# Performance work log

Hardware: AMD Instinct MI355X
Metric: run time of the kernel (lower is better)

The kernel has to match this reference:

```python
import jax, jax.numpy as jnp
import numpy as np
from jax import lax

N_KERNELS = 10000
KS = 9
DILATIONS = (1, 2, 4, 8, 16)   # static dilation groups, 2000 kernels each
GROUP = N_KERNELS // len(DILATIONS)
BN_EPS = 1e-5


def setup_inputs() -> dict:
    key = jax.random.key(0)
    kx, kw, kb, klw = jax.random.split(key, 4)
    B, L, C, n_class = 16, 256, 3, 10
    x_enc = jax.random.normal(kx, (B, L, C), dtype=jnp.float32)
    # ROCKET kernels: normal weights, mean-centered per kernel
    W = jax.random.normal(kw, (N_KERNELS, C, KS), dtype=jnp.float32)
    W = W - W.mean(axis=(1, 2), keepdims=True)
    # ROCKET biases: uniform(-1, 1)
    b = jax.random.uniform(kb, (N_KERNELS,), dtype=jnp.float32) * 2.0 - 1.0
    gamma = jnp.ones((2 * N_KERNELS,), dtype=jnp.float32)
    beta = jnp.zeros((2 * N_KERNELS,), dtype=jnp.float32)
    linW = jax.random.normal(klw, (2 * N_KERNELS, n_class), dtype=jnp.float32) * 0.01
    linB = jnp.zeros((n_class,), dtype=jnp.float32)
    return {"x_enc": x_enc, "W": W, "b": b, "gamma": gamma, "beta": beta,
            "linW": linW, "linB": linB}


def _rocket_features(x, W, b):
    # x: [B, C, L]; W: [N_KERNELS, C, KS]; b: [N_KERNELS]
    feats = []
    dn = ("NCH", "OIH", "NCH")
    for i, d in enumerate(DILATIONS):
        w = W[i * GROUP:(i + 1) * GROUP]                       # [G, C, KS]
        bb = b[i * GROUP:(i + 1) * GROUP]                      # [G]
        y = lax.conv_general_dilated(x, w, window_strides=(1,),
                                     padding="SAME", rhs_dilation=(d,),
                                     dimension_numbers=dn)      # [B, G, L]
        y = y + bb[None, :, None]
        feats.append(y.max(axis=-1))                            # max pooling
        feats.append(jnp.where(y > 0, 1.0, 0.0).mean(axis=-1))  # PPV
    return jnp.concatenate(feats, axis=-1)                      # [B, 2*N_KERNELS]


def reference(x_enc, W, b, gamma, beta, linW, linB):
    x = jnp.transpose(x_enc, (0, 2, 1))        # [B, C, L]
    feat = _rocket_features(x, W, b)           # [B, 20000]
    # BatchNorm1d (training mode: batch statistics, biased variance)
    mu = feat.mean(axis=0)
    var = feat.var(axis=0)
    feat_n = (feat - mu) * lax.rsqrt(var + BN_EPS) * gamma + beta
    return feat_n @ linW + linB                # [B, num_class]
```

## Files before the change

kernel.cpp:

```cpp
#include <hip/hip_runtime.h>
#include <cmath>

#define NK       10000
#define GROUP    2000
#define SEQ_L    256
#define FEAT_DIM 20000
#define NBATCH   16

__launch_bounds__(256)
__global__ void rocket_feat(const float* __restrict__ x_enc,
                            const float* __restrict__ Wk,
                            const float* __restrict__ bias,
                            float* __restrict__ feat)
{
    __shared__ __align__(16) float xs[1152];
    __shared__ float4 red[4][64];

    const int gi   = blockIdx.x >> 4;
    const int sb   = blockIdx.x & 15;
    const int b    = blockIdx.y;
    const int d    = 1 << gi;
    const int Mlen = (SEQ_L >> gi) + 8;
    const int tid  = threadIdx.x;
    const int lane = tid & 63;
    const int wv   = __builtin_amdgcn_readfirstlane(tid >> 6);

    const int dml = d * Mlen;
    for (int idx = tid; idx < 3 * dml; idx += 256) {
        const int c  = idx / dml;
        const int rm = idx - c * dml;
        const int r  = rm / Mlen;
        const int u  = rm - r * Mlen;
        const int t  = r + (u - 4) * d;
        xs[idx] = (t >= 0 && t < SEQ_L) ? x_enc[(b * SEQ_L + t) * 3 + c] : 0.f;
    }

    const int j    = sb * 64 + lane;
    const bool act = (j < 1000);
    const int jj   = act ? j : 0;
    const int n0   = gi * GROUP + jj;
    const int n1   = n0 + 1000;

    float w0[27], w1[27];
#pragma unroll
    for (int q = 0; q < 27; ++q) { w0[q] = Wk[n0 * 27 + q]; w1[q] = Wk[n1 * 27 + q]; }
    const float bs0 = bias[n0];
    const float bs1 = bias[n1];

    __syncthreads();

    float mx0 = -INFINITY, mx1 = -INFINITY;
    float cnt0 = 0.f, cnt1 = 0.f;

    const int mask = (32 >> gi) - 1;
    const int rsh  = 5 - gi;

#pragma unroll
    for (int i = 0; i < 8; ++i) {
        const int om = wv * 8 + i;
        const int r  = om >> rsh;
        const int m0 = (om & mask) << 3;

        float a[8], e[8];
#pragma unroll
        for (int p = 0; p < 8; ++p) { a[p] = bs0; e[p] = bs1; }

#pragma unroll
        for (int c = 0; c < 3; ++c) {
            const float* xc = &xs[(c * d + r) * Mlen + m0];
            float xw[16];
            *(float4*)&xw[0]  = *(const float4*)(xc);
            *(float4*)&xw[4]  = *(const float4*)(xc + 4);
            *(float4*)&xw[8]  = *(const float4*)(xc + 8);
            *(float4*)&xw[12] = *(const float4*)(xc + 12);
#pragma unroll
            for (int k = 0; k < 9; ++k) {
                const float u = w0[c * 9 + k], v = w1[c * 9 + k];
#pragma unroll
                for (int p = 0; p < 8; ++p) {
                    a[p] = fmaf(xw[p + k], u, a[p]);
                    e[p] = fmaf(xw[p + k], v, e[p]);
                }
            }
        }
#pragma unroll
        for (int p = 0; p < 8; ++p) {
            mx0 = fmaxf(mx0, a[p]);  mx1 = fmaxf(mx1, e[p]);
            cnt0 += (a[p] > 0.f) ? 1.f : 0.f;
            cnt1 += (e[p] > 0.f) ? 1.f : 0.f;
        }
    }

    red[wv][lane] = make_float4(mx0, mx1, cnt0, cnt1);
    __syncthreads();

    if (tid < 64 && act) {
        const float4 r0 = red[0][lane], r1 = red[1][lane],
                     r2 = red[2][lane], r3 = red[3][lane];
        const float fmx0 = fmaxf(fmaxf(r0.x, r1.x), fmaxf(r2.x, r3.x));
        const float fmx1 = fmaxf(fmaxf(r0.y, r1.y), fmaxf(r2.y, r3.y));
        const float fc0  = r0.z + r1.z + r2.z + r3.z;
        const float fc1  = r0.w + r1.w + r2.w + r3.w;
        float* fb = feat + b * FEAT_DIM + gi * 4000;
        fb[j]               = fmx0;
        fb[j + 1000]        = fmx1;
        fb[2000 + j]        = fc0 * (1.0f / 256.0f);
        fb[2000 + j + 1000] = fc1 * (1.0f / 256.0f);
    }
}

__launch_bounds__(256)
__global__ void bn_stats(const float* __restrict__ feat,
                         const float* __restrict__ gamma,
                         const float* __restrict__ beta,
                         float* __restrict__ g, float* __restrict__ h)
{
    const int f = blockIdx.x * 256 + threadIdx.x;
    if (f >= FEAT_DIM) return;
    float s = 0.f, ss = 0.f;
#pragma unroll
    for (int b = 0; b < NBATCH; ++b) {
        const float v = feat[b * FEAT_DIM + f];
        s += v;
        ss += v * v;
    }
    const float mu  = s * (1.f / NBATCH);
    const float var = ss * (1.f / NBATCH) - mu * mu;
    const float gg  = gamma[f] * rsqrtf(var + 1e-5f);
    g[f] = gg;
    h[f] = beta[f] - mu * gg;
}

__launch_bounds__(256)
__global__ void gemv_partial(const float* __restrict__ feat,
                             const float* __restrict__ g,
                             const float* __restrict__ h,
                             const float* __restrict__ linW,
                             float* __restrict__ partial)
{
    const int slice = blockIdx.x;
    const int b     = blockIdx.y;
    const int tid   = threadIdx.x;
    const int f0    = slice * 1250;
    const int f1    = f0 + 1250;

    float acc[10];
#pragma unroll
    for (int c = 0; c < 10; ++c) acc[c] = 0.f;

    for (int f = f0 + tid; f < f1; f += 256) {
        const float t = fmaf(feat[b * FEAT_DIM + f], g[f], h[f]);
#pragma unroll
        for (int c = 0; c < 10; ++c) acc[c] = fmaf(t, linW[f * 10 + c], acc[c]);
    }

#pragma unroll
    for (int c = 0; c < 10; ++c)
#pragma unroll
        for (int o = 32; o > 0; o >>= 1) acc[c] += __shfl_down(acc[c], o, 64);

    __shared__ float red[4][10];
    if ((tid & 63) == 0) {
#pragma unroll
        for (int c = 0; c < 10; ++c) red[tid >> 6][c] = acc[c];
    }
    __syncthreads();
    if (tid < 10)
        partial[(b * 16 + slice) * 10 + tid] =
            red[0][tid] + red[1][tid] + red[2][tid] + red[3][tid];
}

__launch_bounds__(160)
__global__ void gemv_final(const float* __restrict__ partial,
                           const float* __restrict__ linB,
                           float* __restrict__ out)
{
    const int tid = threadIdx.x;
    const int b   = tid / 10;
    const int c   = tid - b * 10;
    float s = linB[c];
#pragma unroll
    for (int sl = 0; sl < 16; ++sl) s += partial[(b * 16 + sl) * 10 + c];
    out[tid] = s;
}

extern "C" void kernel_launch(void* const* d_in, const int* in_sizes, int n_in,
                              void* d_out, int out_size, void* d_ws, size_t ws_size,
                              hipStream_t stream) {
    const float* x     = (const float*)d_in[0];
    const float* Wk    = (const float*)d_in[1];
    const float* bias  = (const float*)d_in[2];
    const float* gamma = (const float*)d_in[3];
    const float* beta  = (const float*)d_in[4];
    const float* linW  = (const float*)d_in[5];
    const float* linB  = (const float*)d_in[6];
    float* out = (float*)d_out;

    float* feat    = (float*)d_ws;
    float* g       = feat + NBATCH * FEAT_DIM;
    float* h       = g + FEAT_DIM;
    float* partial = h + FEAT_DIM;

    rocket_feat<<<dim3(80, NBATCH), 256, 0, stream>>>(x, Wk, bias, feat);
    bn_stats<<<dim3((FEAT_DIM + 255) / 256), 256, 0, stream>>>(feat, gamma, beta, g, h);
    gemv_partial<<<dim3(16, NBATCH), 256, 0, stream>>>(feat, g, h, linW, partial);
    gemv_final<<<dim3(1), 160, 0, stream>>>(partial, linB, out);
}
```

Measured before the change: 40.02 us.

## Compute ROCKET convolutions with split-fp16 MFMA and fuse BN stats into GEMV

Recasts each dilation group's convolution as a GEMM: kernel weights are the A operand (27 taps padded to 32), and an im2col matrix of the input, built in shared memory, is the B operand. Both are split into fp16 high and low parts and combined over three MFMA 16x16x32 ops to recover near-fp32 accuracy. Max and PPV are reduced across lanes with shuffles. The batch-norm statistics pass is also folded into the GEMV partial kernel, which removes one launch and the g/h round trip through memory. The split-fp16 scheme drops the low*low term, so results near zero could flip the PPV sign test.

```diff
diff --git a/kernel.cpp b/kernel.cpp
--- a/kernel.cpp
+++ b/kernel.cpp
@@ -7,167 +7,196 @@
 #define FEAT_DIM 20000
 #define NBATCH   16
 
-__launch_bounds__(256)
-__global__ void rocket_feat(const float* __restrict__ x_enc,
+typedef _Float16 half8 __attribute__((ext_vector_type(8)));
+typedef float    f32x4 __attribute__((ext_vector_type(4)));
+
+__launch_bounds__(128)
+__global__ void rocket_mfma(const float* __restrict__ x_enc,
                             const float* __restrict__ Wk,
                             const float* __restrict__ bias,
                             float* __restrict__ feat)
 {
-    __shared__ __align__(16) float xs[1152];
-    __shared__ float4 red[4][64];
-
-    const int gi   = blockIdx.x >> 4;
-    const int sb   = blockIdx.x & 15;
-    const int b    = blockIdx.y;
-    const int d    = 1 << gi;
-    const int Mlen = (SEQ_L >> gi) + 8;
-    const int tid  = threadIdx.x;
-    const int lane = tid & 63;
-    const int wv   = __builtin_amdgcn_readfirstlane(tid >> 6);
-
-    const int dml = d * Mlen;
-    for (int idx = tid; idx < 3 * dml; idx += 256) {
-        const int c  = idx / dml;
-        const int rm = idx - c * dml;
-        const int r  = rm / Mlen;
-        const int u  = rm - r * Mlen;
-        const int t  = r + (u - 4) * d;
-        xs[idx] = (t >= 0 && t < SEQ_L) ? x_enc[(b * SEQ_L + t) * 3 + c] : 0.f;
-    }
-
-    const int j    = sb * 64 + lane;
-    const bool act = (j < 1000);
-    const int jj   = act ? j : 0;
-    const int n0   = gi * GROUP + jj;
-    const int n1   = n0 + 1000;
-
-    float w0[27], w1[27];
-#pragma unroll
-    for (int q = 0; q < 27; ++q) { w0[q] = Wk[n0 * 27 + q]; w1[q] = Wk[n1 * 27 + q]; }
-    const float bs0 = bias[n0];
-    const float bs1 = bias[n1];
-
-    __syncthreads();
-
-    float mx0 = -INFINITY, mx1 = -INFINITY;
-    float cnt0 = 0.f, cnt1 = 0.f;
-
-    const int mask = (32 >> gi) - 1;
-    const int rsh  = 5 - gi;
-
-#pragma unroll
-    for (int i = 0; i < 8; ++i) {
-        const int om = wv * 8 + i;
-        const int r  = om >> rsh;
-        const int m0 = (om & mask) << 3;
-
-        float a[8], e[8];
-#pragma unroll
-        for (int p = 0; p < 8; ++p) { a[p] = bs0; e[p] = bs1; }
-
-#pragma unroll
-        for (int c = 0; c < 3; ++c) {
-            const float* xc = &xs[(c * d + r) * Mlen + m0];
-            float xw[16];
-            *(float4*)&xw[0]  = *(const float4*)(xc);
-            *(float4*)&xw[4]  = *(const float4*)(xc + 4);
-            *(float4*)&xw[8]  = *(const float4*)(xc + 8);
-            *(float4*)&xw[12] = *(const float4*)(xc + 12);
-#pragma unroll
-            for (int k = 0; k < 9; ++k) {
-                const float u = w0[c * 9 + k], v = w1[c * 9 + k];
-#pragma unroll
-                for (int p = 0; p < 8; ++p) {
-                    a[p] = fmaf(xw[p + k], u, a[p]);
-                    e[p] = fmaf(xw[p + k], v, e[p]);
+    __shared__ __align__(16) float     xp[3 * 384];
+    __shared__ __align__(16) _Float16  Bh[4 * 256 * 8];
+    __shared__ __align__(16) _Float16  Bl[4 * 256 * 8];
+
+    const int mt  = blockIdx.x;
+    const int gi  = blockIdx.y;
+    const int b   = blockIdx.z;
+    const int d   = 1 << gi;
+    const int tid = threadIdx.x;
+    const int l   = tid & 63;
+    const int wv  = tid >> 6;
+    const int kb  = l >> 4;
+    const int lr  = l & 15;
+
+    for (int i = tid; i < 3 * 384; i += 128) xp[i] = 0.f;
+    __syncthreads();
+    for (int e = tid; e < SEQ_L * 3; e += 128) {
+        const int t = e / 3;
+        const int c = e - t * 3;
+        xp[c * 384 + 64 + t] = x_enc[(b * SEQ_L + t) * 3 + c];
+    }
+
+    float awf[4][8];
+#pragma unroll
+    for (int tt = 0; tt < 4; ++tt) {
+        const int nl = mt * 128 + wv * 64 + tt * 16 + lr;
+        const int n  = gi * GROUP + (nl < GROUP ? nl : GROUP - 1);
+#pragma unroll
+        for (int j = 0; j < 8; ++j) {
+            const int k = kb * 8 + j;
+            awf[tt][j] = (k < 27) ? Wk[n * 27 + k] : 0.f;
+        }
+    }
+    half8 ahi[4], alo[4];
+#pragma unroll
+    for (int tt = 0; tt < 4; ++tt)
+#pragma unroll
+        for (int j = 0; j < 8; ++j) {
+            const _Float16 h = (_Float16)awf[tt][j];
+            ahi[tt][j] = h;
+            alo[tt][j] = (_Float16)(awf[tt][j] - (float)h);
+        }
+    float bsv[4][4];
+#pragma unroll
+    for (int tt = 0; tt < 4; ++tt)
+#pragma unroll
+        for (int r = 0; r < 4; ++r) {
+            const int nl = mt * 128 + wv * 64 + tt * 16 + kb * 4 + r;
+            bsv[tt][r] = bias[gi * GROUP + (nl < GROUP ? nl : GROUP - 1)];
+        }
+
+    __syncthreads();
+
+    {
+        const int kg = tid >> 5;
+        const int tl = tid & 31;
+#pragma unroll
+        for (int i = 0; i < 8; ++i) {
+            const int t = tl + 32 * i;
+            half8 hv, lv;
+#pragma unroll
+            for (int kk = 0; kk < 8; ++kk) {
+                const int k2 = kg * 8 + kk;
+                float v = 0.f;
+                if (k2 < 27) {
+                    const int c  = (k2 >= 18) ? 2 : (k2 >= 9 ? 1 : 0);
+                    const int k9 = k2 - c * 9;
+                    v = xp[c * 384 + 64 + t + (k9 - 4) * d];
                 }
-            }
-        }
-#pragma unroll
-        for (int p = 0; p < 8; ++p) {
-            mx0 = fmaxf(mx0, a[p]);  mx1 = fmaxf(mx1, e[p]);
-            cnt0 += (a[p] > 0.f) ? 1.f : 0.f;
-            cnt1 += (e[p] > 0.f) ? 1.f : 0.f;
-        }
-    }
-
-    red[wv][lane] = make_float4(mx0, mx1, cnt0, cnt1);
-    __syncthreads();
-
-    if (tid < 64 && act) {
-        const float4 r0 = red[0][lane], r1 = red[1][lane],
-                     r2 = red[2][lane], r3 = red[3][lane];
-        const float fmx0 = fmaxf(fmaxf(r0.x, r1.x), fmaxf(r2.x, r3.x));
-        const float fmx1 = fmaxf(fmaxf(r0.y, r1.y), fmaxf(r2.y, r3.y));
-        const float fc0  = r0.z + r1.z + r2.z + r3.z;
-        const float fc1  = r0.w + r1.w + r2.w + r3.w;
+                const _Float16 h = (_Float16)v;
+                hv[kk] = h;
+                lv[kk] = (_Float16)(v - (float)h);
+            }
+            *(half8*)&Bh[(kg * 256 + t) * 8] = hv;
+            *(half8*)&Bl[(kg * 256 + t) * 8] = lv;
+        }
+    }
+    __syncthreads();
+
+    float mx[4][4], cnt[4][4];
+#pragma unroll
+    for (int tt = 0; tt < 4; ++tt)
+#pragma unroll
+        for (int r = 0; r < 4; ++r) { mx[tt][r] = -INFINITY; cnt[tt][r] = 0.f; }
+
+#pragma unroll
+    for (int ch = 0; ch < 16; ++ch) {
+        const int t = ch * 16 + lr;
+        const half8 bh = *(const half8*)&Bh[(kb * 256 + t) * 8];
+        const half8 bl = *(const half8*)&Bl[(kb * 256 + t) * 8];
+#pragma unroll
+        for (int tt = 0; tt < 4; ++tt) {
+            f32x4 acc = {0.f, 0.f, 0.f, 0.f};
+            acc = __builtin_amdgcn_mfma_f32_16x16x32_f16(ahi[tt], bh, acc, 0, 0, 0);
+            acc = __builtin_amdgcn_mfma_f32_16x16x32_f16(alo[tt], bh, acc, 0, 0, 0);
+            acc = __builtin_amdgcn_mfma_f32_16x16x32_f16(ahi[tt], bl, acc, 0, 0, 0);
+#pragma unroll
+            for (int r = 0; r < 4; ++r) {
+                const float y = acc[r] + bsv[tt][r];
+                mx[tt][r]  = fmaxf(mx[tt][r], y);
+                cnt[tt][r] += (y > 0.f) ? 1.f : 0.f;
+            }
+        }
+    }
+
+#pragma unroll
+    for (int tt = 0; tt < 4; ++tt)
+#pragma unroll
+        for (int r = 0; r < 4; ++r) {
+#pragma unroll
+            for (int m = 1; m < 16; m <<= 1) {
+                mx[tt][r]  = fmaxf(mx[tt][r], __shfl_xor(mx[tt][r], m));
+                cnt[tt][r] += __shfl_xor(cnt[tt][r], m);
+            }
+        }
+
+    if (lr == 0) {
         float* fb = feat + b * FEAT_DIM + gi * 4000;
-        fb[j]               = fmx0;
-        fb[j + 1000]        = fmx1;
-        fb[2000 + j]        = fc0 * (1.0f / 256.0f);
-        fb[2000 + j + 1000] = fc1 * (1.0f / 256.0f);
+#pragma unroll
+        for (int tt = 0; tt < 4; ++tt)
+#pragma unroll
+            for (int r = 0; r < 4; ++r) {
+                const int nl = mt * 128 + wv * 64 + tt * 16 + kb * 4 + r;
+                if (nl < GROUP) {
+                    fb[nl]         = mx[tt][r];
+                    fb[2000 + nl]  = cnt[tt][r] * (1.0f / 256.0f);
+                }
+            }
     }
 }
 
 __launch_bounds__(256)
-__global__ void bn_stats(const float* __restrict__ feat,
-                         const float* __restrict__ gamma,
-                         const float* __restrict__ beta,
-                         float* __restrict__ g, float* __restrict__ h)
+__global__ void bn_gemv(const float* __restrict__ feat,
+                        const float* __restrict__ gamma,
+                        const float* __restrict__ beta,
+                        const float* __restrict__ linW,
+                        float* __restrict__ partial)
 {
-    const int f = blockIdx.x * 256 + threadIdx.x;
-    if (f >= FEAT_DIM) return;
-    float s = 0.f, ss = 0.f;
-#pragma unroll
-    for (int b = 0; b < NBATCH; ++b) {
-        const float v = feat[b * FEAT_DIM + f];
-        s += v;
-        ss += v * v;
-    }
-    const float mu  = s * (1.f / NBATCH);
-    const float var = ss * (1.f / NBATCH) - mu * mu;
-    const float gg  = gamma[f] * rsqrtf(var + 1e-5f);
-    g[f] = gg;
-    h[f] = beta[f] - mu * gg;
-}
-
-__launch_bounds__(256)
-__global__ void gemv_partial(const float* __restrict__ feat,
-                             const float* __restrict__ g,
-                             const float* __restrict__ h,
-                             const float* __restrict__ linW,
-                             float* __restrict__ partial)
-{
-    const int slice = blockIdx.x;
-    const int b     = blockIdx.y;
-    const int tid   = threadIdx.x;
-    const int f0    = slice * 1250;
-    const int f1    = f0 + 1250;
-
+    __shared__ float gs[625], hs[625];
+    const int sl  = blockIdx.x;
+    const int f0  = sl * 625;
+    const int tid = threadIdx.x;
+
+    for (int i = tid; i < 625; i += 256) {
+        const int f = f0 + i;
+        float s = 0.f, ss = 0.f;
+#pragma unroll
+        for (int b = 0; b < NBATCH; ++b) {
+            const float v = feat[b * FEAT_DIM + f];
+            s += v; ss += v * v;
+        }
+        const float mu  = s * (1.f / NBATCH);
+        const float var = ss * (1.f / NBATCH) - mu * mu;
+        const float gg  = gamma[f] * rsqrtf(var + 1e-5f);
+        gs[i] = gg;
+        hs[i] = beta[f] - mu * gg;
+    }
+    __syncthreads();
+
+    const int bb = tid >> 4;
+    const int ft = tid & 15;
     float acc[10];
 #pragma unroll
     for (int c = 0; c < 10; ++c) acc[c] = 0.f;
 
-    for (int f = f0 + tid; f < f1; f += 256) {
-        const float t = fmaf(feat[b * FEAT_DIM + f], g[f], h[f]);
-#pragma unroll
-        for (int c = 0; c < 10; ++c) acc[c] = fmaf(t, linW[f * 10 + c], acc[c]);
-    }
-
+    for (int i = ft; i < 625; i += 16) {
+        const int f = f0 + i;
+        const float tv = fmaf(feat[bb * FEAT_DIM + f], gs[i], hs[i]);
+#pragma unroll
+        for (int c = 0; c < 10; ++c) acc[c] = fmaf(tv, linW[f * 10 + c], acc[c]);
+    }
 #pragma unroll
     for (int c = 0; c < 10; ++c)
 #pragma unroll
-        for (int o = 32; o > 0; o >>= 1) acc[c] += __shfl_down(acc[c], o, 64);
-
-    __shared__ float red[4][10];
-    if ((tid & 63) == 0) {
-#pragma unroll
-        for (int c = 0; c < 10; ++c) red[tid >> 6][c] = acc[c];
-    }
-    __syncthreads();
-    if (tid < 10)
-        partial[(b * 16 + slice) * 10 + tid] =
-            red[0][tid] + red[1][tid] + red[2][tid] + red[3][tid];
+        for (int m = 1; m < 16; m <<= 1) acc[c] += __shfl_xor(acc[c], m);
+
+    if (ft == 0) {
+#pragma unroll
+        for (int c = 0; c < 10; ++c)
+            partial[(sl * NBATCH + bb) * 10 + c] = acc[c];
+    }
 }
 
 __launch_bounds__(160)
@@ -176,11 +205,10 @@
                            float* __restrict__ out)
 {
     const int tid = threadIdx.x;
-    const int b   = tid / 10;
-    const int c   = tid - b * 10;
+    const int c   = tid % 10;
     float s = linB[c];
 #pragma unroll
-    for (int sl = 0; sl < 16; ++sl) s += partial[(b * 16 + sl) * 10 + c];
+    for (int sl = 0; sl < 32; ++sl) s += partial[sl * 160 + tid];
     out[tid] = s;
 }
 
@@ -197,12 +225,9 @@
     float* out = (float*)d_out;
 
     float* feat    = (float*)d_ws;
-    float* g       = feat + NBATCH * FEAT_DIM;
-    float* h       = g + FEAT_DIM;
-    float* partial = h + FEAT_DIM;
-
-    rocket_feat<<<dim3(80, NBATCH), 256, 0, stream>>>(x, Wk, bias, feat);
-    bn_stats<<<dim3((FEAT_DIM + 255) / 256), 256, 0, stream>>>(feat, gamma, beta, g, h);
-    gemv_partial<<<dim3(16, NBATCH), 256, 0, stream>>>(feat, g, h, linW, partial);
+    float* partial = feat + NBATCH * FEAT_DIM;
+
+    rocket_mfma<<<dim3(16, 5, NBATCH), 128, 0, stream>>>(x, Wk, bias, feat);
+    bn_gemv<<<dim3(32), 256, 0, stream>>>(feat, gamma, beta, linW, partial);
     gemv_final<<<dim3(1), 160, 0, stream>>>(partial, linB, out);
 }
```

After: 42.93 us. 1.07x slower.
